# Optimization experiments

Measured on AMD Instinct MI355X. Metric: run time of the kernel, lower is better.

## Reference

```python
import jax, jax.numpy as jnp
import numpy as np

B, S, HID = 2, 2048, 2048
H, KV, D = 16, 4, 128
ROT = 64           # partial rotary dim (= cos.shape[-1])
EMB = 128          # router embedding dim
TAU, BASE = 0.4, 3.0
EPS = 1e-6


def rotate_half(x):
    h = x.shape[-1] // 2
    return jnp.concatenate([-x[..., h:], x[..., :h]], axis=-1)


def rmsnorm(x, w, eps=EPS):
    # Qwen3.5: zero-init weight, (1 + w) scaling, compute in fp32
    xf = x.astype(jnp.float32)
    o = xf * jax.lax.rsqrt(jnp.mean(xf * xf, axis=-1, keepdims=True) + eps)
    return (o * (1.0 + w.astype(jnp.float32))).astype(x.dtype)


def _rope_tables():
    inv_freq = 1.0 / (10000.0 ** (np.arange(0, ROT, 2, dtype=np.float32) / ROT))
    t = np.arange(S, dtype=np.float32)
    freqs = np.outer(t, inv_freq)                 # [S, ROT/2]
    emb = np.concatenate([freqs, freqs], axis=-1)  # [S, ROT]
    cos = np.broadcast_to(np.cos(emb), (B, S, ROT)).copy()
    sin = np.broadcast_to(np.sin(emb), (B, S, ROT)).copy()
    return jnp.asarray(cos), jnp.asarray(sin)


def setup_inputs() -> dict:
    key = jax.random.key(0)
    ks = jax.random.split(key, 10)
    sc = 0.02
    cos, sin = _rope_tables()
    return {
        "hidden_states": jax.random.normal(ks[0], (B, S, HID), jnp.float32),
        "cos": cos,
        "sin": sin,
        # projection weights stored as [in, out] (torch Linear weight transposed)
        "Wq": jax.random.normal(ks[1], (HID, H * D * 2), jnp.float32) * sc,
        "Wk": jax.random.normal(ks[2], (HID, KV * D), jnp.float32) * sc,
        "Wv": jax.random.normal(ks[3], (HID, KV * D), jnp.float32) * sc,
        "Wo": jax.random.normal(ks[4], (H * D, HID), jnp.float32) * sc,
        "q_norm_w": jnp.zeros((D,), jnp.float32),
        "k_norm_w": jnp.zeros((D,), jnp.float32),
        "Wr": jax.random.normal(ks[5], (HID, EMB), jnp.float32) * sc,   # router linear
        "Wd": jax.random.normal(ks[6], (EMB, D), jnp.float32) * sc,     # router decoder
        "ln_g": jnp.ones((EMB,), jnp.float32),
        "ln_b": jnp.zeros((EMB,), jnp.float32),
        "rnn_state": jnp.zeros((EMB,), jnp.float32),
    }


def _forward(hidden_states, cos, sin, Wq, Wk, Wv, Wo, q_norm_w, k_norm_w,
             Wr, Wd, ln_g, ln_b, rnn_state):
    b, s, _ = hidden_states.shape
    # doubled q_proj -> query + gate
    qkv = jnp.einsum('bsh,hd->bsd', hidden_states, Wq).reshape(b, s, H, 2 * D)
    q, gate = qkv[..., :D], qkv[..., D:]
    gate = gate.reshape(b, s, H * D)
    k = jnp.einsum('bsh,hd->bsd', hidden_states, Wk).reshape(b, s, KV, D)
    v = jnp.einsum('bsh,hd->bsd', hidden_states, Wv).reshape(b, s, KV, D)
    # per-head RMSNorm then [b, h, s, d]
    q = rmsnorm(q, q_norm_w).transpose(0, 2, 1, 3)
    k = rmsnorm(k, k_norm_w).transpose(0, 2, 1, 3)
    v = v.transpose(0, 2, 1, 3)

    # --- head-dim router (gumbel-sigmoid, straight-through hard round) ---
    emb = jnp.einsum('bsh,he->bse', hidden_states, Wr) + rnn_state
    mu = jnp.mean(emb, -1, keepdims=True)
    var = jnp.mean((emb - mu) ** 2, -1, keepdims=True)
    ln = (emb - mu) * jax.lax.rsqrt(var + 1e-5) * ln_g + ln_b
    logits = jnp.einsum('bse,ed->bsd', jax.nn.gelu(ln, approximate=False), Wd)
    gum = -jnp.log(jax.random.exponential(jax.random.key(42), logits.shape, jnp.float32))
    y_soft = jax.nn.sigmoid((logits + gum + BASE) / TAU)
    binary = jax.lax.stop_gradient(jnp.round(y_soft) - y_soft) + y_soft  # [b, s, D]
    mask = binary[:, None, :, :]  # broadcast over heads: [b, 1, s, D]

    q = q * mask
    k = k * mask

    # partial RoPE on first ROT dims (qk_index=None training path)
    c = cos[:, None, :, :]
    si = sin[:, None, :, :]
    def rope(x):
        xr, xp = x[..., :ROT], x[..., ROT:]
        return jnp.concatenate([xr * c + rotate_half(xr) * si, xp], axis=-1)
    q = rope(q)
    k = rope(k)

    # GQA: repeat kv heads
    rep = H // KV
    k = jnp.repeat(k, rep, axis=1)
    v = jnp.repeat(v, rep, axis=1)

    scores = jnp.einsum('bhqd,bhkd->bhqk', q, k) / np.sqrt(D).astype(np.float32)
    causal = jnp.tril(jnp.ones((s, s), bool))
    scores = jnp.where(causal, scores, jnp.finfo(jnp.float32).min)
    attn = jax.nn.softmax(scores.astype(jnp.float32), axis=-1).astype(q.dtype)
    out = jnp.einsum('bhqk,bhkd->bhqd', attn, v)
    out = out.transpose(0, 2, 1, 3).reshape(b, s, H * D)
    out = out * jax.nn.sigmoid(gate)   # output gate
    return jnp.einsum('bsd,dh->bsh', out, Wo)


def reference(hidden_states, cos, sin, Wq, Wk, Wv, Wo, q_norm_w, k_norm_w,
              Wr, Wd, ln_g, ln_b, rnn_state):
    return _forward(hidden_states, cos, sin, Wq, Wk, Wv, Wo, q_norm_w, k_norm_w,
                    Wr, Wd, ln_g, ln_b, rnn_state)
```

## Files before the change

kernel.cpp:

```cpp
#include <hip/hip_runtime.h>
#include <math.h>

typedef __bf16 bf16;
typedef bf16 bf16x8 __attribute__((ext_vector_type(8)));
typedef bf16 bf16x4 __attribute__((ext_vector_type(4)));
typedef float f32x4 __attribute__((ext_vector_type(4)));

#define BB 2
#define SS 2048
#define NPROJ 5248
#define QSCALE (0.08838834764831845f * 1.4426950408889634f)
#define USHIFT 32.0f

__device__ __forceinline__ float waveAllReduceSum(float v) {
#pragma unroll
  for (int o = 1; o < 64; o <<= 1) v += __shfl_xor(v, o, 64);
  return v;
}

__device__ __forceinline__ int xcd_swz(int orig, int nwg) {
  return (orig & 7) * (nwg >> 3) + (orig >> 3);
}

__device__ __forceinline__ void gload16(const bf16* g, bf16* l) {
  __builtin_amdgcn_global_load_lds((const __attribute__((address_space(1))) void*)g,
                                   (__attribute__((address_space(3))) void*)l, 16, 0, 0);
}

__device__ __forceinline__ void do_transpose(bf16 (*tile)[72], const float* __restrict__ W,
                                             bf16* __restrict__ WT, int K, int N, int rowOff,
                                             int bx, int by, int t) {
  int n0 = bx * 64, k0 = by * 64;
  {
    int c4 = (t & 15) * 4, r = t >> 4;
#pragma unroll
    for (int p = 0; p < 4; p++) {
      int row = p * 16 + r;
      float4 v = *reinterpret_cast<const float4*>(W + (size_t)(k0 + row) * N + n0 + c4);
      bf16x4 o = {(bf16)v.x, (bf16)v.y, (bf16)v.z, (bf16)v.w};
      *reinterpret_cast<bf16x4*>(&tile[row][c4]) = o;
    }
  }
  __syncthreads();
  {
    int ln = t & 7, n = t >> 3;
#pragma unroll
    for (int p = 0; p < 2; p++) {
      int nn = p * 32 + n;
      bf16x8 o;
#pragma unroll
      for (int j = 0; j < 8; j++) o[j] = tile[ln * 8 + j][nn];
      *reinterpret_cast<bf16x8*>(WT + (size_t)(rowOff + n0 + nn) * K + k0 + ln * 8) = o;
    }
  }
  __syncthreads();
}

__global__ __launch_bounds__(256) void prep_weights(const float* __restrict__ hidden,
                                                    const float* __restrict__ Wq,
                                                    const float* __restrict__ Wk,
                                                    const float* __restrict__ Wv,
                                                    const float* __restrict__ Wr,
                                                    const float* __restrict__ Wo,
                                                    bf16* __restrict__ hb,
                                                    bf16* __restrict__ WTall,
                                                    bf16* __restrict__ WoT) {
  __shared__ bf16 tile[64][72];
  int id = blockIdx.x, t = threadIdx.x;
  if (id < 4096) {
    int i = (id * 256 + t) * 8;
    float4 v0 = *reinterpret_cast<const float4*>(hidden + i);
    float4 v1 = *reinterpret_cast<const float4*>(hidden + i + 4);
    bf16x8 o = {(bf16)v0.x, (bf16)v0.y, (bf16)v0.z, (bf16)v0.w,
                (bf16)v1.x, (bf16)v1.y, (bf16)v1.z, (bf16)v1.w};
    *reinterpret_cast<bf16x8*>(hb + i) = o;
    return;
  }
  int id2 = id - 4096;
  if (id2 < 2048) { do_transpose(tile, Wq, WTall, 2048, 4096, 0, id2 & 63, id2 >> 6, t); return; }
  id2 -= 2048;
  if (id2 < 256) { do_transpose(tile, Wk, WTall, 2048, 512, 4096, id2 & 7, id2 >> 3, t); return; }
  id2 -= 256;
  if (id2 < 256) { do_transpose(tile, Wv, WTall, 2048, 512, 4608, id2 & 7, id2 >> 3, t); return; }
  id2 -= 256;
  if (id2 < 64) { do_transpose(tile, Wr, WTall, 2048, 128, 5120, id2 & 1, id2 >> 1, t); return; }
  id2 -= 64;
  do_transpose(tile, Wo, WoT, 2048, 2048, 0, id2 & 31, id2 >> 5, t);
}

template <typename CT>
__global__ __launch_bounds__(256) void gemm_bt(const bf16* __restrict__ A,
                                               const bf16* __restrict__ Bt,
                                               CT* __restrict__ C, int M, int N, int K) {
  __shared__ bf16 lA[128 * 64];
  __shared__ bf16 lB[128 * 64];
  const int nbx = N >> 7;
  int wg = xcd_swz(blockIdx.x, gridDim.x);
  int bx = wg % nbx, by = wg / nbx;
  const int t = threadIdx.x;
  const int l = t & 63, w = t >> 6;
  const int wr = w >> 1, wc = w & 1;
  const int lr = l & 15, lhi = l >> 4;

  f32x4 acc[4][4];
#pragma unroll
  for (int m = 0; m < 4; m++)
#pragma unroll
    for (int n = 0; n < 4; n++) acc[m][n] = f32x4{0.f, 0.f, 0.f, 0.f};

  const int rowA0 = by * 128, rowB0 = bx * 128;
  const int nkt = K >> 6;
  for (int kt = 0; kt < nkt; ++kt) {
    __syncthreads();
#pragma unroll
    for (int it = 0; it < 4; ++it) {
      int slot = it * 256 + t;
      int row = slot >> 3, sl = slot & 7;
      gload16(A + (size_t)(rowA0 + row) * K + kt * 64 + ((sl ^ (row & 7)) << 3), lA + slot * 8);
      gload16(Bt + (size_t)(rowB0 + row) * K + kt * 64 + ((sl ^ (row & 7)) << 3), lB + slot * 8);
    }
    __syncthreads();
#pragma unroll
    for (int kc = 0; kc < 2; ++kc) {
      bf16x8 af[4], bg[4];
#pragma unroll
      for (int m = 0; m < 4; m++) {
        int row = wr * 64 + m * 16 + lr;
        af[m] = *reinterpret_cast<const bf16x8*>((char*)lA + row * 128 + (((kc * 4 + lhi) ^ (row & 7)) << 4));
      }
#pragma unroll
      for (int n = 0; n < 4; n++) {
        int row = wc * 64 + n * 16 + lr;
        bg[n] = *reinterpret_cast<const bf16x8*>((char*)lB + row * 128 + (((kc * 4 + lhi) ^ (row & 7)) << 4));
      }
      __builtin_amdgcn_s_setprio(1);
#pragma unroll
      for (int m = 0; m < 4; m++)
#pragma unroll
        for (int n = 0; n < 4; n++)
          acc[m][n] = __builtin_amdgcn_mfma_f32_16x16x32_bf16(af[m], bg[n], acc[m][n], 0, 0, 0);
      __builtin_amdgcn_s_setprio(0);
    }
  }
#pragma unroll
  for (int m = 0; m < 4; m++)
#pragma unroll
    for (int n = 0; n < 4; n++)
#pragma unroll
      for (int r = 0; r < 4; r++) {
        int grow = rowA0 + wr * 64 + m * 16 + lhi * 4 + r;
        int gcol = rowB0 + wc * 64 + n * 16 + lr;
        C[(size_t)grow * N + gcol] = (CT)acc[m][n][r];
      }
}

__device__ __forceinline__ unsigned rotl32(unsigned x, int r) { return (x << r) | (x >> (32 - r)); }

__device__ __forceinline__ float gumbel42(unsigned i) {
  const unsigned half = (unsigned)(BB * SS * 128) / 2u;
  unsigned x0, x1;
  int word;
  if (i < half) { x0 = i; x1 = i + half; word = 0; }
  else          { x0 = i - half; x1 = i; word = 1; }
  const unsigned k0 = 0u, k1 = 42u;
  const unsigned k2 = k0 ^ k1 ^ 0x1BD11BDAu;
  x0 += k0; x1 += k1;
#define TF_R(r) { x0 += x1; x1 = rotl32(x1, r); x1 ^= x0; }
  TF_R(13) TF_R(15) TF_R(26) TF_R(6)
  x0 += k1; x1 += k2 + 1u;
  TF_R(17) TF_R(29) TF_R(16) TF_R(24)
  x0 += k2; x1 += k0 + 2u;
  TF_R(13) TF_R(15) TF_R(26) TF_R(6)
  x0 += k0; x1 += k1 + 3u;
  TF_R(17) TF_R(29) TF_R(16) TF_R(24)
  x0 += k1; x1 += k2 + 4u;
  TF_R(13) TF_R(15) TF_R(26) TF_R(6)
  x0 += k2; x1 += k0 + 5u;
#undef TF_R
  unsigned bits = word ? x1 : x0;
  float u = __uint_as_float((bits >> 9) | 0x3f800000u) - 1.0f;
  float ex = -log1pf(-u);
  return -logf(ex);
}

__global__ __launch_bounds__(128) void mask_kernel(const bf16* __restrict__ qkva,
                                                   const float* __restrict__ rnn,
                                                   const float* __restrict__ lng,
                                                   const float* __restrict__ lnb,
                                                   const float* __restrict__ Wd,
                                                   bf16* __restrict__ maskb) {
  int row = blockIdx.x;
  int t = threadIdx.x;
  int l = t & 63, w = t >> 6;
  __shared__ float redm[2], redv[2], gsh[128];
  float e = (float)qkva[(size_t)row * NPROJ + 5120 + t] + rnn[t];
  float s1 = waveAllReduceSum(e);
  if (l == 0) redm[w] = s1;
  __syncthreads();
  float mu = (redm[0] + redm[1]) * (1.0f / 128.0f);
  float dv = (e - mu) * (e - mu);
  float s2 = waveAllReduceSum(dv);
  if (l == 0) redv[w] = s2;
  __syncthreads();
  float var = (redv[0] + redv[1]) * (1.0f / 128.0f);
  float ln = (e - mu) * rsqrtf(var + 1e-5f) * lng[t] + lnb[t];
  float g = 0.5f * ln * (1.0f + erff(ln * 0.7071067811865475f));
  gsh[t] = g;
  __syncthreads();
  float logit = 0.f;
#pragma unroll 8
  for (int e2 = 0; e2 < 128; e2++) logit += gsh[e2] * Wd[e2 * 128 + t];
  float gum = gumbel42((unsigned)(row * 128 + t));
  float x = (logit + gum + 3.0f) * 2.5f;
  float y = 1.0f / (1.0f + expf(-x));
  maskb[(size_t)row * 128 + t] = (bf16)rintf(y);
}

__global__ __launch_bounds__(256) void qkv_prep(const bf16* __restrict__ qkva,
                                                const bf16* __restrict__ maskb,
                                                const float* __restrict__ kw,
                                                const float* __restrict__ cosT,
                                                const float* __restrict__ sinT,
                                                bf16* __restrict__ wk,
                                                bf16* __restrict__ wvt) {
  int id = blockIdx.x, t = threadIdx.x;
  if (id < 1024) {
    int g = t >> 4, ln = t & 15;
    int hr = id * 16 + g;
    int kv = hr & 3, row = hr >> 2;
    int b = row >> 11, s = row & 2047;
    const bf16* kp = qkva + (size_t)row * NPROJ + 4096 + kv * 128 + ln * 8;
    bf16x8 k8 = *reinterpret_cast<const bf16x8*>(kp);
    bf16x8 m8 = *reinterpret_cast<const bf16x8*>(maskb + (size_t)row * 128 + ln * 8);
    float kf[8], ss = 0.f;
#pragma unroll
    for (int j = 0; j < 8; j++) { kf[j] = (float)k8[j]; ss += kf[j] * kf[j]; }
#pragma unroll
    for (int o = 1; o < 16; o <<= 1) ss += __shfl_xor(ss, o, 16);
    float rinv = rsqrtf(ss * (1.0f / 128.0f) + 1e-6f);
    alignas(16) float wv[8];
    const float4* kw4 = reinterpret_cast<const float4*>(kw);
    *reinterpret_cast<float4*>(&wv[0]) = kw4[ln * 2];
    *reinterpret_cast<float4*>(&wv[4]) = kw4[ln * 2 + 1];
    float km[8];
#pragma unroll
    for (int j = 0; j < 8; j++) km[j] = kf[j] * rinv * (1.0f + wv[j]) * (float)m8[j];
    alignas(16) float c8[8], s8[8];
    if (ln < 8) {
      const float4* c4 = reinterpret_cast<const float4*>(cosT + (size_t)row * 64);
      const float4* sn4 = reinterpret_cast<const float4*>(sinT + (size_t)row * 64);
      *reinterpret_cast<float4*>(&c8[0]) = c4[ln * 2];
      *reinterpret_cast<float4*>(&c8[4]) = c4[ln * 2 + 1];
      *reinterpret_cast<float4*>(&s8[0]) = sn4[ln * 2];
      *reinterpret_cast<float4*>(&s8[4]) = sn4[ln * 2 + 1];
    }
    float po[8];
#pragma unroll
    for (int j = 0; j < 8; j++) po[j] = __shfl_xor(km[j], 4, 16);
    bf16x8 ok;
#pragma unroll
    for (int j = 0; j < 8; j++) {
      float ov;
      if (ln < 4) ov = km[j] * c8[j] - po[j] * s8[j];
      else if (ln < 8) ov = km[j] * c8[j] + po[j] * s8[j];
      else ov = km[j];
      ok[j] = (bf16)ov;
    }
    *reinterpret_cast<bf16x8*>(wk + ((size_t)((b * 4 + kv) * 2048 + s)) * 128 + ln * 8) = ok;
    return;
  }
  {
    __shared__ bf16 tl[64][72];
    int vb = id - 1024;
    int dt = vb & 1;
    int st = (vb >> 1) & 31;
    int bkv = vb >> 6;
    int b = bkv >> 2, kv = bkv & 3;
    int tx = t & 63, ty = t >> 6;
    int s0 = st * 64, d0 = dt * 64;
#pragma unroll
    for (int i = 0; i < 16; i++) {
      int srow = ty + i * 4;
      tl[srow][tx] = qkva[(size_t)(b * 2048 + s0 + srow) * NPROJ + 4608 + kv * 128 + d0 + tx];
    }
    __syncthreads();
#pragma unroll
    for (int i = 0; i < 16; i++) {
      int drow = ty + i * 4;
      wvt[(size_t)((b * 4 + kv) * 128 + d0 + drow) * 2048 + s0 + tx] = tl[tx][drow];
    }
  }
}

__global__ __launch_bounds__(512) void attn_kernel(const bf16* __restrict__ qkva,
                                                   const bf16* __restrict__ wk,
                                                   const bf16* __restrict__ wvt,
                                                   const bf16* __restrict__ maskb,
                                                   const float* __restrict__ qw,
                                                   const float* __restrict__ cosT,
                                                   const float* __restrict__ sinT,
                                                   bf16* __restrict__ wattn) {
  __shared__ bf16 lK[2][64 * 128];
  __shared__ bf16 lV[2][128 * 64];
  __shared__ bf16 lP[8][16 * 64];
  int bid = blockIdx.x;
  int grp = bid & 7;
  int b = grp >> 2, kvh = grp & 3;
  int g32 = bid >> 3;
  int pp = g32 & 7;
  int h = kvh * 4 + (g32 >> 3);
  int bh = b * 16 + h;
  int t = threadIdx.x, l = t & 63, w = t >> 6;
  int lr = l & 15, lhi = l >> 4;

  const bf16* kbase = wk + (size_t)((b * 4 + kvh) * 2048) * 128;
  const bf16* vbase = wvt + (size_t)((b * 4 + kvh) * 128) * 2048;
  char* pb = (char*)(&lP[w][0]);

  const int n0 = 2 * pp + 2;

  auto stage = [&](int buf, int tt) {
#pragma unroll
    for (int it = 0; it < 2; ++it) {
      int slot = it * 512 + t;
      int row = slot >> 4, sl = slot & 15;
      gload16(kbase + (size_t)(tt * 64 + row) * 128 + ((sl ^ (row & 7)) << 3), lK[buf] + slot * 8);
      int row2 = slot >> 3, sl2 = slot & 7;
      gload16(vbase + (size_t)row2 * 2048 + tt * 64 + ((sl2 ^ (row2 & 7)) << 3), lV[buf] + slot * 8);
    }
  };

  bf16x8 aq[4];
  f32x4 oacc[8];
  float l_run;
  int qb128 = pp;

  auto load_q = [&](int qbv) {
    int srow = qbv * 128 + w * 16 + lr;
    int grow = b * 2048 + srow;
    const bf16* qp = qkva + (size_t)grow * NPROJ + h * 256;
    int dbase = lhi * 8;
    float qf[4][8];
    float ss = 0.f;
#pragma unroll
    for (int kc = 0; kc < 4; kc++) {
      bf16x8 v = *reinterpret_cast<const bf16x8*>(qp + kc * 32 + dbase);
#pragma unroll
      for (int j = 0; j < 8; j++) { qf[kc][j] = (float)v[j]; ss += qf[kc][j] * qf[kc][j]; }
    }
    ss += __shfl_xor(ss, 16, 64);
    ss += __shfl_xor(ss, 32, 64);
    float rinv = rsqrtf(ss * (1.0f / 128.0f) + 1e-6f);
    const bf16* mrow = maskb + (size_t)grow * 128;
    float qm[4][8];
#pragma unroll
    for (int kc = 0; kc < 4; kc++) {
      bf16x8 m8 = *reinterpret_cast<const bf16x8*>(mrow + kc * 32 + dbase);
      float4 wa = *reinterpret_cast<const float4*>(qw + kc * 32 + dbase);
      float4 wb = *reinterpret_cast<const float4*>(qw + kc * 32 + dbase + 4);
      alignas(16) float wv[8];
      *reinterpret_cast<float4*>(&wv[0]) = wa;
      *reinterpret_cast<float4*>(&wv[4]) = wb;
#pragma unroll
      for (int j = 0; j < 8; j++) qm[kc][j] = qf[kc][j] * rinv * (1.0f + wv[j]) * (float)m8[j];
    }
    const float* crow = cosT + (size_t)grow * 64;
    const float* srw = sinT + (size_t)grow * 64;
    alignas(16) float c0[8], c1[8], s0[8], s1[8];
    *reinterpret_cast<float4*>(&c0[0]) = *reinterpret_cast<const float4*>(crow + dbase);
    *reinterpret_cast<float4*>(&c0[4]) = *reinterpret_cast<const float4*>(crow + dbase + 4);
    *reinterpret_cast<float4*>(&c1[0]) = *reinterpret_cast<const float4*>(crow + 32 + dbase);
    *reinterpret_cast<float4*>(&c1[4]) = *reinterpret_cast<const float4*>(crow + 32 + dbase + 4);
    *reinterpret_cast<float4*>(&s0[0]) = *reinterpret_cast<const float4*>(srw + dbase);
    *reinterpret_cast<float4*>(&s0[4]) = *reinterpret_cast<const float4*>(srw + dbase + 4);
    *reinterpret_cast<float4*>(&s1[0]) = *reinterpret_cast<const float4*>(srw + 32 + dbase);
    *reinterpret_cast<float4*>(&s1[4]) = *reinterpret_cast<const float4*>(srw + 32 + dbase + 4);
#pragma unroll
    for (int j = 0; j < 8; j++) {
      float o0 = qm[0][j] * c0[j] - qm[1][j] * s0[j];
      float o1 = qm[1][j] * c1[j] + qm[0][j] * s1[j];
      aq[0][j] = (bf16)(o0 * QSCALE);
      aq[1][j] = (bf16)(o1 * QSCALE);
      aq[2][j] = (bf16)(qm[2][j] * QSCALE);
      aq[3][j] = (bf16)(qm[3][j] * QSCALE);
    }
  };

  load_q(pp);
#pragma unroll
  for (int db = 0; db < 8; db++) oacc[db] = f32x4{0.f, 0.f, 0.f, 0.f};
  l_run = 0.f;

  stage(0, 0);
  __syncthreads();
  int cur = 0;

  for (int i = 0; i < 34; ++i) {
    int tt = (i < n0) ? i : i - n0;
    if (i + 1 < 34) {
      int tn = (i + 1 < n0) ? (i + 1) : (i + 1 - n0);
      stage(cur ^ 1, tn);
    }
    int qrow0 = qb128 * 128 + w * 16;

    f32x4 sacc[4];
#pragma unroll
    for (int j = 0; j < 4; j++) sacc[j] = f32x4{0.f, 0.f, 0.f, 0.f};
    __builtin_amdgcn_s_setprio(1);
#pragma unroll
    for (int kc = 0; kc < 4; kc++)
#pragma unroll
      for (int j = 0; j < 4; j++) {
        int row = j * 16 + lr;
        bf16x8 ak = *reinterpret_cast<const bf16x8*>((char*)lK[cur] + row * 256 + (((kc * 4 + lhi) ^ (row & 7)) << 4));
        sacc[j] = __builtin_amdgcn_mfma_f32_16x16x32_bf16(ak, aq[kc], sacc[j], 0, 0, 0);
      }
    __builtin_amdgcn_s_setprio(0);

    if (tt * 64 + 63 > qrow0) {
      int qrow_g = qrow0 + lr;
#pragma unroll
      for (int j = 0; j < 4; j++)
#pragma unroll
        for (int r = 0; r < 4; r++) {
          int kg = tt * 64 + j * 16 + lhi * 4 + r;
          if (kg > qrow_g) sacc[j][r] = -1e30f;
        }
    }

    float p[4][4];
    float rs = 0.f;
#pragma unroll
    for (int j = 0; j < 4; j++) {
#pragma unroll
      for (int r = 0; r < 4; r++) {
        float pv = exp2f(sacc[j][r] - USHIFT);
        p[j][r] = pv;
        rs += pv;
      }
    }
    l_run += rs;

#pragma unroll
    for (int j = 0; j < 4; j++) {
      bf16x4 p4 = {(bf16)p[j][0], (bf16)p[j][1], (bf16)p[j][2], (bf16)p[j][3]};
      *reinterpret_cast<bf16x4*>(pb + lr * 128 + ((j * 32 + lhi * 8) ^ ((lr & 7) << 4))) = p4;
    }
    bf16x8 pa[2];
#pragma unroll
    for (int kc2 = 0; kc2 < 2; kc2++)
      pa[kc2] = *reinterpret_cast<const bf16x8*>(pb + lr * 128 + ((kc2 * 64 + lhi * 16) ^ ((lr & 7) << 4)));
    __builtin_amdgcn_s_setprio(1);
#pragma unroll
    for (int kc2 = 0; kc2 < 2; kc2++)
#pragma unroll
      for (int db = 0; db < 8; db++) {
        int row = db * 16 + lr;
        bf16x8 bv = *reinterpret_cast<const bf16x8*>((char*)lV[cur] + row * 128 + (((kc2 * 4 + lhi) ^ (row & 7)) << 4));
        oacc[db] = __builtin_amdgcn_mfma_f32_16x16x32_bf16(pa[kc2], bv, oacc[db], 0, 0, 0);
      }
    __builtin_amdgcn_s_setprio(0);

    if (i == n0 - 1 || i == 33) {
      float lsum = l_run;
      lsum += __shfl_xor(lsum, 16, 64);
      lsum += __shfl_xor(lsum, 32, 64);
      float linv[4];
#pragma unroll
      for (int r = 0; r < 4; r++) linv[r] = 1.0f / __shfl(lsum, lhi * 4 + r, 64);
#pragma unroll
      for (int r = 0; r < 4; r++) {
        int srow = qb128 * 128 + w * 16 + lhi * 4 + r;
        const bf16* grow_p = qkva + (size_t)(b * 2048 + srow) * NPROJ + h * 256 + 128;
#pragma unroll
        for (int db = 0; db < 8; db++) {
          int dcol = db * 16 + lr;
          float graw = (float)grow_p[dcol];
          float g = 1.0f / (1.0f + expf(-graw));
          float ov = oacc[db][r] * linv[r] * g;
          wattn[(size_t)(b * 2048 + srow) * 2048 + h * 128 + dcol] = (bf16)ov;
        }
      }
      if (i == n0 - 1) {
        qb128 = 15 - pp;
        load_q(qb128);
#pragma unroll
        for (int db = 0; db < 8; db++) oacc[db] = f32x4{0.f, 0.f, 0.f, 0.f};
        l_run = 0.f;
      }
    }

    __syncthreads();
    cur ^= 1;
  }
}

extern "C" void kernel_launch(void* const* d_in, const int* in_sizes, int n_in,
                              void* d_out, int out_size, void* d_ws, size_t ws_size,
                              hipStream_t stream) {
  const float* hidden = (const float*)d_in[0];
  const float* cosT = (const float*)d_in[1];
  const float* sinT = (const float*)d_in[2];
  const float* Wq = (const float*)d_in[3];
  const float* Wk = (const float*)d_in[4];
  const float* Wv = (const float*)d_in[5];
  const float* Wo = (const float*)d_in[6];
  const float* qw = (const float*)d_in[7];
  const float* kw = (const float*)d_in[8];
  const float* Wr = (const float*)d_in[9];
  const float* Wd = (const float*)d_in[10];
  const float* lng = (const float*)d_in[11];
  const float* lnb = (const float*)d_in[12];
  const float* rnn = (const float*)d_in[13];
  float* out = (float*)d_out;

  char* p = (char*)d_ws;
  auto alloc = [&](size_t bytes) { char* r = p; p += (bytes + 255) & ~(size_t)255; return r; };
  bf16* hb    = (bf16*)alloc((size_t)4096 * 2048 * 2);
  bf16* WTall = (bf16*)alloc((size_t)NPROJ * 2048 * 2);
  bf16* WoT   = (bf16*)alloc((size_t)2048 * 2048 * 2);
  bf16* qkva  = (bf16*)alloc((size_t)4096 * NPROJ * 2);
  bf16* maskb = (bf16*)alloc((size_t)4096 * 128 * 2);
  bf16* wkb   = (bf16*)alloc((size_t)2 * 4 * 2048 * 128 * 2);
  bf16* wvtb  = (bf16*)alloc((size_t)2 * 4 * 128 * 2048 * 2);
  bf16* wab   = (bf16*)alloc((size_t)4096 * 2048 * 2);
  if ((size_t)(p - (char*)d_ws) > ws_size) return;

  prep_weights<<<7744, 256, 0, stream>>>(hidden, Wq, Wk, Wv, Wr, Wo, hb, WTall, WoT);

  gemm_bt<bf16><<<41 * 32, 256, 0, stream>>>(hb, WTall, qkva, 4096, NPROJ, 2048);

  mask_kernel<<<4096, 128, 0, stream>>>(qkva, rnn, lng, lnb, Wd, maskb);
  qkv_prep<<<1536, 256, 0, stream>>>(qkva, maskb, kw, cosT, sinT, wkb, wvtb);

  attn_kernel<<<256, 512, 0, stream>>>(qkva, wkb, wvtb, maskb, qw, cosT, sinT, wab);

  gemm_bt<float><<<16 * 32, 256, 0, stream>>>(wab, WoT, out, 4096, 2048, 2048);
}
```

Before: 268.5 us.

## Split fused projection GEMM into large-tile Q/gate GEMM and small KV/router GEMM

The single fused 4096x5248 projection GEMM is split in two. A new 256x256-tile, 512-thread, double-buffered gemm_qg kernel handles the 4096 query/gate columns, and the existing 128-tile kernel handles the 1152 K/V/router columns. The outputs now go to separate buffers with their own strides, and the downstream kernels are re-indexed to match. The larger tiles aim for more data reuse and better MFMA utilisation on the dominant GEMM, and the split also removes the awkward 41-column-tile grid. The costs are an extra kernel launch and a 256-workgroup grid, which may not fill every CU.

New measurement: 266.0 us. About the same (-0.9%).

```diff
diff --git a/kernel.cpp b/kernel.cpp
--- a/kernel.cpp
+++ b/kernel.cpp
@@ -8,7 +8,7 @@
 
 #define BB 2
 #define SS 2048
-#define NPROJ 5248
+#define NKVE 1152
 #define QSCALE (0.08838834764831845f * 1.4426950408889634f)
 #define USHIFT 32.0f
 
@@ -151,6 +151,96 @@
         int grow = rowA0 + wr * 64 + m * 16 + lhi * 4 + r;
         int gcol = rowB0 + wc * 64 + n * 16 + lr;
         C[(size_t)grow * N + gcol] = (CT)acc[m][n][r];
+      }
+}
+
+__global__ __launch_bounds__(512, 2) void gemm_qg(const bf16* __restrict__ A,
+                                                  const bf16* __restrict__ Bt,
+                                                  bf16* __restrict__ Cq) {
+  __shared__ bf16 lA[2][256 * 64];
+  __shared__ bf16 lB[2][256 * 64];
+  int wg = xcd_swz(blockIdx.x, 256);
+  int bx = wg & 15, by = wg >> 4;
+  const int t = threadIdx.x;
+  const int l = t & 63, w = t >> 6;
+  const int wm = w >> 2, wn = w & 3;
+  const int lr = l & 15, lhi = l >> 4;
+  const int K = 2048;
+
+  f32x4 acc[8][4];
+#pragma unroll
+  for (int m = 0; m < 8; m++)
+#pragma unroll
+    for (int n = 0; n < 4; n++) acc[m][n] = f32x4{0.f, 0.f, 0.f, 0.f};
+
+  const int rowA0 = by * 256, rowB0 = bx * 256;
+
+  auto stage = [&](int buf, int kt) {
+#pragma unroll
+    for (int it = 0; it < 4; ++it) {
+      int slot = it * 512 + t;
+      int row = slot >> 3, sl = slot & 7;
+      gload16(A + (size_t)(rowA0 + row) * K + kt * 64 + ((sl ^ (row & 7)) << 3), lA[buf] + slot * 8);
+      gload16(Bt + (size_t)(rowB0 + row) * K + kt * 64 + ((sl ^ (row & 7)) << 3), lB[buf] + slot * 8);
+    }
+  };
+
+  stage(0, 0);
+  stage(1, 1);
+
+  for (int kt = 0; kt < 32; ++kt) {
+    int cur = kt & 1;
+    if (kt < 31) {
+      asm volatile("s_waitcnt vmcnt(8)" ::: "memory");
+    } else {
+      asm volatile("s_waitcnt vmcnt(0)" ::: "memory");
+    }
+    __builtin_amdgcn_sched_barrier(0);
+    __builtin_amdgcn_s_barrier();
+    __builtin_amdgcn_sched_barrier(0);
+
+#pragma unroll
+    for (int ks = 0; ks < 2; ++ks) {
+      bf16x8 bg[4];
+#pragma unroll
+      for (int n = 0; n < 4; n++) {
+        int row = wn * 64 + n * 16 + lr;
+        bg[n] = *reinterpret_cast<const bf16x8*>((char*)lB[cur] + row * 128 + (((ks * 4 + lhi) ^ (row & 7)) << 4));
+      }
+#pragma unroll
+      for (int mh = 0; mh < 2; ++mh) {
+        bf16x8 af[4];
+#pragma unroll
+        for (int m = 0; m < 4; m++) {
+          int row = wm * 128 + (mh * 4 + m) * 16 + lr;
+          af[m] = *reinterpret_cast<const bf16x8*>((char*)lA[cur] + row * 128 + (((ks * 4 + lhi) ^ (row & 7)) << 4));
+        }
+        __builtin_amdgcn_s_setprio(1);
+#pragma unroll
+        for (int m = 0; m < 4; m++)
+#pragma unroll
+          for (int n = 0; n < 4; n++)
+            acc[mh * 4 + m][n] = __builtin_amdgcn_mfma_f32_16x16x32_bf16(af[m], bg[n], acc[mh * 4 + m][n], 0, 0, 0);
+        __builtin_amdgcn_s_setprio(0);
+      }
+    }
+
+    asm volatile("s_waitcnt lgkmcnt(0)" ::: "memory");
+    __builtin_amdgcn_sched_barrier(0);
+    __builtin_amdgcn_s_barrier();
+    __builtin_amdgcn_sched_barrier(0);
+    if (kt + 2 < 32) stage(cur, kt + 2);
+  }
+
+#pragma unroll
+  for (int m = 0; m < 8; m++)
+#pragma unroll
+    for (int n = 0; n < 4; n++)
+#pragma unroll
+      for (int r = 0; r < 4; r++) {
+        int grow = rowA0 + wm * 128 + m * 16 + lhi * 4 + r;
+        int gcol = rowB0 + wn * 64 + n * 16 + lr;
+        Cq[(size_t)grow * 4096 + gcol] = (bf16)acc[m][n][r];
       }
 }
 
@@ -183,7 +273,7 @@
   return -logf(ex);
 }
 
-__global__ __launch_bounds__(128) void mask_kernel(const bf16* __restrict__ qkva,
+__global__ __launch_bounds__(128) void mask_kernel(const bf16* __restrict__ kve,
                                                    const float* __restrict__ rnn,
                                                    const float* __restrict__ lng,
                                                    const float* __restrict__ lnb,
@@ -193,7 +283,7 @@
   int t = threadIdx.x;
   int l = t & 63, w = t >> 6;
   __shared__ float redm[2], redv[2], gsh[128];
-  float e = (float)qkva[(size_t)row * NPROJ + 5120 + t] + rnn[t];
+  float e = (float)kve[(size_t)row * NKVE + 1024 + t] + rnn[t];
   float s1 = waveAllReduceSum(e);
   if (l == 0) redm[w] = s1;
   __syncthreads();
@@ -216,7 +306,7 @@
   maskb[(size_t)row * 128 + t] = (bf16)rintf(y);
 }
 
-__global__ __launch_bounds__(256) void qkv_prep(const bf16* __restrict__ qkva,
+__global__ __launch_bounds__(256) void qkv_prep(const bf16* __restrict__ kve,
                                                 const bf16* __restrict__ maskb,
                                                 const float* __restrict__ kw,
                                                 const float* __restrict__ cosT,
@@ -229,7 +319,7 @@
     int hr = id * 16 + g;
     int kv = hr & 3, row = hr >> 2;
     int b = row >> 11, s = row & 2047;
-    const bf16* kp = qkva + (size_t)row * NPROJ + 4096 + kv * 128 + ln * 8;
+    const bf16* kp = kve + (size_t)row * NKVE + kv * 128 + ln * 8;
     bf16x8 k8 = *reinterpret_cast<const bf16x8*>(kp);
     bf16x8 m8 = *reinterpret_cast<const bf16x8*>(maskb + (size_t)row * 128 + ln * 8);
     float kf[8], ss = 0.f;
@@ -281,7 +371,7 @@
 #pragma unroll
     for (int i = 0; i < 16; i++) {
       int srow = ty + i * 4;
-      tl[srow][tx] = qkva[(size_t)(b * 2048 + s0 + srow) * NPROJ + 4608 + kv * 128 + d0 + tx];
+      tl[srow][tx] = kve[(size_t)(b * 2048 + s0 + srow) * NKVE + 512 + kv * 128 + d0 + tx];
     }
     __syncthreads();
 #pragma unroll
@@ -292,7 +382,7 @@
   }
 }
 
-__global__ __launch_bounds__(512) void attn_kernel(const bf16* __restrict__ qkva,
+__global__ __launch_bounds__(512) void attn_kernel(const bf16* __restrict__ qg,
                                                    const bf16* __restrict__ wk,
                                                    const bf16* __restrict__ wvt,
                                                    const bf16* __restrict__ maskb,
@@ -338,7 +428,7 @@
   auto load_q = [&](int qbv) {
     int srow = qbv * 128 + w * 16 + lr;
     int grow = b * 2048 + srow;
-    const bf16* qp = qkva + (size_t)grow * NPROJ + h * 256;
+    const bf16* qp = qg + (size_t)grow * 4096 + h * 256;
     int dbase = lhi * 8;
     float qf[4][8];
     float ss = 0.f;
@@ -471,7 +561,7 @@
 #pragma unroll
       for (int r = 0; r < 4; r++) {
         int srow = qb128 * 128 + w * 16 + lhi * 4 + r;
-        const bf16* grow_p = qkva + (size_t)(b * 2048 + srow) * NPROJ + h * 256 + 128;
+        const bf16* grow_p = qg + (size_t)(b * 2048 + srow) * 4096 + h * 256 + 128;
 #pragma unroll
         for (int db = 0; db < 8; db++) {
           int dcol = db * 16 + lr;
@@ -517,9 +607,10 @@
   char* p = (char*)d_ws;
   auto alloc = [&](size_t bytes) { char* r = p; p += (bytes + 255) & ~(size_t)255; return r; };
   bf16* hb    = (bf16*)alloc((size_t)4096 * 2048 * 2);
-  bf16* WTall = (bf16*)alloc((size_t)NPROJ * 2048 * 2);
+  bf16* WTall = (bf16*)alloc((size_t)5248 * 2048 * 2);
   bf16* WoT   = (bf16*)alloc((size_t)2048 * 2048 * 2);
-  bf16* qkva  = (bf16*)alloc((size_t)4096 * NPROJ * 2);
+  bf16* qgb   = (bf16*)alloc((size_t)4096 * 4096 * 2);
+  bf16* kveb  = (bf16*)alloc((size_t)4096 * NKVE * 2);
   bf16* maskb = (bf16*)alloc((size_t)4096 * 128 * 2);
   bf16* wkb   = (bf16*)alloc((size_t)2 * 4 * 2048 * 128 * 2);
   bf16* wvtb  = (bf16*)alloc((size_t)2 * 4 * 128 * 2048 * 2);
@@ -528,12 +619,15 @@
 
   prep_weights<<<7744, 256, 0, stream>>>(hidden, Wq, Wk, Wv, Wr, Wo, hb, WTall, WoT);
 
-  gemm_bt<bf16><<<41 * 32, 256, 0, stream>>>(hb, WTall, qkva, 4096, NPROJ, 2048);
-
-  mask_kernel<<<4096, 128, 0, stream>>>(qkva, rnn, lng, lnb, Wd, maskb);
-  qkv_prep<<<1536, 256, 0, stream>>>(qkva, maskb, kw, cosT, sinT, wkb, wvtb);
-
-  attn_kernel<<<256, 512, 0, stream>>>(qkva, wkb, wvtb, maskb, qw, cosT, sinT, wab);
+  gemm_bt<bf16><<<288, 256, 0, stream>>>(hb, WTall + (size_t)4096 * 2048, kveb, 4096, NKVE, 2048);
+
+  mask_kernel<<<4096, 128, 0, stream>>>(kveb, rnn, lng, lnb, Wd, maskb);
+
+  gemm_qg<<<256, 512, 0, stream>>>(hb, WTall, qgb);
+
+  qkv_prep<<<1536, 256, 0, stream>>>(kveb, maskb, kw, cosT, sinT, wkb, wvtb);
+
+  attn_kernel<<<256, 512, 0, stream>>>(qgb, wkb, wvtb, maskb, qw, cosT, sinT, wab);
 
   gemm_bt<float><<<16 * 32, 256, 0, stream>>>(wab, WoT, out, 4096, 2048, 2048);
 }
```
